# Performance work log

Measured on AMD Instinct MI355X. Metric: run time of the kernel, lower is better.

The kernel has to match this reference:

```python
import jax, jax.numpy as jnp
import numpy as np

B, S, D, H = 2, 2048, 2048, 16
HD = D // H  # 128


def _rope_tables(seq_len, dim, base=10000.0):
    inv_freq = 1.0 / (base ** (jnp.arange(0, dim, 2, dtype=jnp.float32) / dim))
    t = jnp.arange(seq_len, dtype=jnp.float32)
    freqs = jnp.outer(t, inv_freq)  # [S, dim/2]
    return jnp.cos(freqs), jnp.sin(freqs)


def _apply_rotary(x, cos, sin):
    # x: [B, S, H, HD]; cos/sin: [S, HD/2] -> broadcast [1, S, 1, HD/2]
    half = x.shape[-1] // 2
    x1, x2 = x[..., :half], x[..., half:]
    c = cos[None, :, None, :]
    s = sin[None, :, None, :]
    return jnp.concatenate([x1 * c - x2 * s, x1 * s + x2 * c], axis=-1)


def setup_inputs() -> dict:
    key = jax.random.key(0)
    ks = jax.random.split(key, 5)
    x = jax.random.normal(ks[0], (B, S, D), dtype=jnp.float32)
    Wq = jax.random.normal(ks[1], (D, D), dtype=jnp.float32) * 0.02
    Wk = jax.random.normal(ks[2], (D, D), dtype=jnp.float32) * 0.02
    Wv = jax.random.normal(ks[3], (D, D), dtype=jnp.float32) * 0.02
    Wo = jax.random.normal(ks[4], (D, D), dtype=jnp.float32) * 0.02
    mask = jnp.tril(jnp.ones((S, S), dtype=jnp.int32))[None, None]  # [1,1,S,S] causal
    return {"x": x, "mask": mask, "Wq": Wq, "Wk": Wk, "Wv": Wv, "Wo": Wo}


def reference(x, mask, Wq, Wk, Wv, Wo):
    b, s, d = x.shape
    # nn.Linear(bias=False): y = x @ W.T
    q = (x @ Wq.T).reshape(b, s, H, HD)
    k = (x @ Wk.T).reshape(b, s, H, HD)
    v = (x @ Wv.T).reshape(b, s, H, HD)
    cos, sin = _rope_tables(s, HD)
    q = _apply_rotary(q, cos, sin)
    k = _apply_rotary(k, cos, sin)
    # -> [B, H, S, HD]
    q = q.transpose(0, 2, 1, 3)
    k = k.transpose(0, 2, 1, 3)
    v = v.transpose(0, 2, 1, 3)
    scores = jnp.einsum('bhqd,bhkd->bhqk', q, k) / jnp.sqrt(jnp.float32(HD))
    scores = jnp.where(mask == 0, -jnp.inf, scores)
    attn = jax.nn.softmax(scores, axis=-1)
    out = jnp.einsum('bhqk,bhkd->bhqd', attn, v)
    out = out.transpose(0, 2, 1, 3).reshape(b, s, d)
    return out @ Wo.T
```

## Files before the change

### kernel.cpp

```cpp
#include <hip/hip_runtime.h>
#include <hip/hip_bf16.h>

typedef __attribute__((ext_vector_type(8))) short short8;
typedef __attribute__((ext_vector_type(4))) short s4;
typedef __attribute__((ext_vector_type(4))) float f32x4;

#define S_TOK 2048

__device__ __forceinline__ float b2f(ushort u) {
  union { unsigned i; float f; } v; v.i = ((unsigned)u) << 16; return v.f;
}
__device__ __forceinline__ ushort f2b(float f) {
  __hip_bfloat16 h = __float2bfloat16(f);
  union { __hip_bfloat16 h; ushort u; } v; v.h = h; return v.u;
}

__device__ __forceinline__ void async_load16(const void* g, void* l) {
  __builtin_amdgcn_global_load_lds(
      (const __attribute__((address_space(1))) unsigned int*)g,
      (__attribute__((address_space(3))) unsigned int*)l, 16, 0, 0);
}

__device__ __forceinline__ void wg_barrier() {
  __asm__ volatile("" ::: "memory");
  __builtin_amdgcn_s_barrier();
  __asm__ volatile("" ::: "memory");
}

__device__ const int QT_OF[40] = {0,1,2,3, 4,4,5,5,6,6,7,7, 8,8,8,9,9,9,10,10,10,11,11,11,
                                  12,12,12,12,13,13,13,13,14,14,14,14,15,15,15,15};
__device__ const int C_OF[40]  = {0,0,0,0, 0,1,0,1,0,1,0,1, 0,1,2,0,1,2,0,1,2,0,1,2,
                                  0,1,2,3,0,1,2,3,0,1,2,3,0,1,2,3};
__device__ const int S0_OF[16] = {0,1,2,3,4,6,8,10,12,15,18,21,24,28,32,36};
__device__ const int NC_OF[16] = {1,1,1,1,2,2,2,2,3,3,3,3,4,4,4,4};
__device__ const int SORD[40] = {3,4,6,8,10,11,12,13,15,16,18,19,21,22,23,24,25,26,28,29,
                                 30,32,33,34,36,37,38,39, 2,9,20,35, 1,7,17,31, 0,5,14,27};

__global__ __launch_bounds__(256) void cvt_f32_bf16(const float* __restrict__ in,
                                                    ushort* __restrict__ out, int n) {
  int i = (blockIdx.x * 256 + threadIdx.x) * 4;
  if (i < n) {
    float4 v = *(const float4*)(in + i);
    ushort4 o;
    o.x = f2b(v.x); o.y = f2b(v.y); o.z = f2b(v.z); o.w = f2b(v.w);
    *(ushort4*)(out + i) = o;
  }
}

__global__ __launch_bounds__(256) void cvt_w4(const float* __restrict__ w0,
                                              const float* __restrict__ w1,
                                              const float* __restrict__ w2,
                                              const float* __restrict__ w3,
                                              ushort* __restrict__ out, int n) {
  const float* src = blockIdx.y == 0 ? w0 : blockIdx.y == 1 ? w1 : blockIdx.y == 2 ? w2 : w3;
  int i = (blockIdx.x * 256 + threadIdx.x) * 4;
  if (i < n) {
    float4 v = *(const float4*)(src + i);
    ushort4 o;
    o.x = f2b(v.x); o.y = f2b(v.y); o.z = f2b(v.z); o.w = f2b(v.w);
    *(ushort4*)(out + (size_t)blockIdx.y * n + i) = o;
  }
}

template <bool OUTF32>
__global__ __launch_bounds__(512, 2) void gemm256(const ushort* __restrict__ A,
                                                  const ushort* __restrict__ Bw,
                                                  void* __restrict__ Cv,
                                                  int lda, int ldb, int ldc) {
  __shared__ __align__(16) ushort As[4][256 * 32];
  __shared__ __align__(16) ushort Bs[4][256 * 32];
  const int tid  = threadIdx.x;
  const int lane = tid & 63;
  const int w    = tid >> 6;
  const int quad = lane >> 4;
  const int l15  = lane & 15;
  const int m0 = blockIdx.x * 256;
  const int n0 = blockIdx.y * 256;
  const int wm = (w & 1) * 128;
  const int wn = (w >> 1) * 64;

  f32x4 acc[8][4];
  #pragma unroll
  for (int i = 0; i < 8; ++i)
    #pragma unroll
    for (int j = 0; j < 4; ++j) acc[i][j] = (f32x4){0.f, 0.f, 0.f, 0.f};

  auto stage = [&](int t, int j) {
    const int r = t & 3;
    const int s = tid + j * 512;
    const int row = s >> 2, qp = s & 3;
    const int kof = (qp ^ ((row >> 1) & 3)) * 8;
    const int k0 = t * 32;
    async_load16(A  + (size_t)(m0 + row) * lda + k0 + kof, &As[r][s * 8]);
    async_load16(Bw + (size_t)(n0 + row) * ldb + k0 + kof, &Bs[r][s * 8]);
  };

  stage(0, 0); stage(0, 1);
  stage(1, 0); stage(1, 1);
  stage(2, 0); stage(2, 1);
  __asm__ volatile("s_waitcnt vmcnt(8)" ::: "memory");
  wg_barrier();

  constexpr int nT = 64;
  #pragma unroll 1
  for (int u = 0; u < nT; ++u) {
    const ushort* At = As[u & 3];
    const ushort* Bt = Bs[u & 3];
    short8 afr[4], bfr[4];

    #pragma unroll
    for (int ni = 0; ni < 4; ++ni) {
      int row = wn + ni * 16 + l15;
      bfr[ni] = *(const short8*)&Bt[(row * 4 + (quad ^ ((row >> 1) & 3))) * 8];
    }
    #pragma unroll
    for (int mi = 0; mi < 4; ++mi) {
      int row = wm + mi * 16 + l15;
      afr[mi] = *(const short8*)&At[(row * 4 + (quad ^ ((row >> 1) & 3))) * 8];
    }
    if (u + 3 < nT) stage(u + 3, 0);
    wg_barrier();
    __asm__ volatile("s_waitcnt lgkmcnt(0)" ::: "memory");
    __builtin_amdgcn_s_setprio(1);
    #pragma unroll
    for (int mi = 0; mi < 4; ++mi)
      #pragma unroll
      for (int ni = 0; ni < 4; ++ni)
        acc[mi][ni] = __builtin_amdgcn_mfma_f32_16x16x32_bf16(afr[mi], bfr[ni], acc[mi][ni], 0, 0, 0);
    __builtin_amdgcn_s_setprio(0);
    wg_barrier();

    #pragma unroll
    for (int mi = 0; mi < 4; ++mi) {
      int row = wm + 64 + mi * 16 + l15;
      afr[mi] = *(const short8*)&At[(row * 4 + (quad ^ ((row >> 1) & 3))) * 8];
    }
    if (u + 3 < nT) stage(u + 3, 1);
    wg_barrier();
    __asm__ volatile("s_waitcnt lgkmcnt(0)" ::: "memory");
    __builtin_amdgcn_s_setprio(1);
    #pragma unroll
    for (int mi = 0; mi < 4; ++mi)
      #pragma unroll
      for (int ni = 0; ni < 4; ++ni)
        acc[4 + mi][ni] = __builtin_amdgcn_mfma_f32_16x16x32_bf16(afr[mi], bfr[ni], acc[4 + mi][ni], 0, 0, 0);
    __builtin_amdgcn_s_setprio(0);
    if (u + 3 < nT)      { __asm__ volatile("s_waitcnt vmcnt(8)" ::: "memory"); }
    else if (u + 2 < nT) { __asm__ volatile("s_waitcnt vmcnt(4)" ::: "memory"); }
    else if (u + 1 < nT) { __asm__ volatile("s_waitcnt vmcnt(0)" ::: "memory"); }
    wg_barrier();
  }

  #pragma unroll
  for (int mi = 0; mi < 8; ++mi)
    #pragma unroll
    for (int ni = 0; ni < 4; ++ni)
      #pragma unroll
      for (int r = 0; r < 4; ++r) {
        int rr = m0 + wm + mi * 16 + quad * 4 + r;
        int cc = n0 + wn + ni * 16 + l15;
        if constexpr (OUTF32)
          ((float*)Cv)[(size_t)rr * ldc + cc] = acc[mi][ni][r];
        else
          ((ushort*)Cv)[(size_t)rr * ldc + cc] = f2b(acc[mi][ni][r]);
      }
}

template <int BM, int BN, bool OUTF32>
__global__ __launch_bounds__(512, 2) void gemm_mn(const ushort* __restrict__ A,
                                                  const ushort* __restrict__ Bw,
                                                  void* __restrict__ Cv,
                                                  int lda, int ldb, int ldc) {
  constexpr int LA = BM / 128;
  constexpr int LB = BN / 128;
  constexpr int MI = BM / 32;
  constexpr int NI = BN / 64;
  static_assert(LA + LB == 3, "vmcnt literals assume 3 loads/thread/tile");
  __shared__ __align__(16) ushort As[4][BM * 32];
  __shared__ __align__(16) ushort Bs[4][BN * 32];
  const int tid  = threadIdx.x;
  const int lane = tid & 63;
  const int w    = tid >> 6;
  const int quad = lane >> 4;
  const int l15  = lane & 15;
  const int m0 = blockIdx.x * BM;
  const int n0 = blockIdx.y * BN;
  const int wm = (w & 1) * (BM / 2);
  const int wn = (w >> 1) * (BN / 4);

  f32x4 acc[MI][NI];
  #pragma unroll
  for (int i = 0; i < MI; ++i)
    #pragma unroll
    for (int j = 0; j < NI; ++j) acc[i][j] = (f32x4){0.f, 0.f, 0.f, 0.f};

  auto stage = [&](int t) {
    const int r = t & 3;
    const int k0 = t * 32;
    #pragma unroll
    for (int ja = 0; ja < LA; ++ja) {
      int s = tid + ja * 512;
      int row = s >> 2, qp = s & 3;
      int kof = (qp ^ ((row >> 1) & 3)) * 8;
      async_load16(A + (size_t)(m0 + row) * lda + k0 + kof, &As[r][s * 8]);
    }
    #pragma unroll
    for (int jb = 0; jb < LB; ++jb) {
      int s = tid + jb * 512;
      int row = s >> 2, qp = s & 3;
      int kof = (qp ^ ((row >> 1) & 3)) * 8;
      async_load16(Bw + (size_t)(n0 + row) * ldb + k0 + kof, &Bs[r][s * 8]);
    }
  };

  stage(0); stage(1); stage(2);
  __asm__ volatile("s_waitcnt vmcnt(6)" ::: "memory");
  wg_barrier();

  constexpr int nT = 64;
  #pragma unroll 1
  for (int u = 0; u < nT; ++u) {
    const ushort* At = As[u & 3];
    const ushort* Bt = Bs[u & 3];
    short8 afr[MI], bfr[NI];
    #pragma unroll
    for (int ni = 0; ni < NI; ++ni) {
      int row = wn + ni * 16 + l15;
      bfr[ni] = *(const short8*)&Bt[(row * 4 + (quad ^ ((row >> 1) & 3))) * 8];
    }
    #pragma unroll
    for (int mi = 0; mi < MI; ++mi) {
      int row = wm + mi * 16 + l15;
      afr[mi] = *(const short8*)&At[(row * 4 + (quad ^ ((row >> 1) & 3))) * 8];
    }
    if (u + 3 < nT) stage(u + 3);
    wg_barrier();
    __asm__ volatile("s_waitcnt lgkmcnt(0)" ::: "memory");
    __builtin_amdgcn_s_setprio(1);
    #pragma unroll
    for (int mi = 0; mi < MI; ++mi)
      #pragma unroll
      for (int ni = 0; ni < NI; ++ni)
        acc[mi][ni] = __builtin_amdgcn_mfma_f32_16x16x32_bf16(afr[mi], bfr[ni], acc[mi][ni], 0, 0, 0);
    __builtin_amdgcn_s_setprio(0);
    if (u + 3 < nT)      { __asm__ volatile("s_waitcnt vmcnt(6)" ::: "memory"); }
    else if (u + 2 < nT) { __asm__ volatile("s_waitcnt vmcnt(3)" ::: "memory"); }
    else if (u + 1 < nT) { __asm__ volatile("s_waitcnt vmcnt(0)" ::: "memory"); }
    wg_barrier();
  }

  #pragma unroll
  for (int mi = 0; mi < MI; ++mi)
    #pragma unroll
    for (int ni = 0; ni < NI; ++ni)
      #pragma unroll
      for (int r = 0; r < 4; ++r) {
        int rr = m0 + wm + mi * 16 + quad * 4 + r;
        int cc = n0 + wn + ni * 16 + l15;
        if constexpr (OUTF32)
          ((float*)Cv)[(size_t)rr * ldc + cc] = acc[mi][ni][r];
        else
          ((ushort*)Cv)[(size_t)rr * ldc + cc] = f2b(acc[mi][ni][r]);
      }
}

__global__ __launch_bounds__(256) void rope_k(ushort* __restrict__ QK) {
  const int t = blockIdx.x * 256 + threadIdx.x;
  const int j = t & 63;
  const int h = (t >> 6) & 15;
  const int row = t >> 10;
  const int pos = row & (S_TOK - 1);
  const float invf = __expf(-0.14391156831212787f * (float)j);
  const float ph = (float)pos * invf;
  float sn, cs;
  __sincosf(ph, &sn, &cs);
  size_t base = (size_t)row * 4096 + 2048 + h * 128 + j;
  float y1 = b2f(QK[base]);
  float y2 = b2f(QK[base + 64]);
  QK[base]      = f2b(y1 * cs - y2 * sn);
  QK[base + 64] = f2b(y1 * sn + y2 * cs);
}

__global__ __launch_bounds__(256, 2) void attn_chunk(const ushort* __restrict__ QK,
                                                     const ushort* __restrict__ Vt,
                                                     ushort* __restrict__ Opart,
                                                     float* __restrict__ Ml) {
  __shared__ __align__(16) ushort Ks[2][8192];
  __shared__ __align__(16) ushort Vs[2][8192];
  const int s = SORD[blockIdx.x];
  const int h = blockIdx.y, b = blockIdx.z;
  const int qt = QT_OF[s], c = C_OF[s];
  const int q0 = qt * 128;
  const int t0 = c * 8, tend = min(t0 + 8, 2 * qt + 2);
  const int slot = (b * 16 + h) * 40 + s;
  const int tid = threadIdx.x, lane = tid & 63, w = tid >> 6;
  const int quad = lane >> 4, l15 = lane & 15;
  const size_t rowbase = (size_t)b * S_TOK;
  const float scale = 0.08838834764831845f;

  short8 qf[2][4];
  #pragma unroll
  for (int m = 0; m < 2; ++m)
    #pragma unroll
    for (int ks = 0; ks < 4; ++ks)
      qf[m][ks] = *(const short8*)(QK + (rowbase + q0 + w * 32 + m * 16 + l15) * 4096
                                   + h * 128 + ks * 32 + quad * 8);

  #pragma unroll
  for (int m = 0; m < 2; ++m) {
    const int pos = (q0 + w * 32 + m * 16 + l15) & (S_TOK - 1);
    #pragma unroll
    for (int ks = 0; ks < 2; ++ks)
      #pragma unroll
      for (int j = 0; j < 8; ++j) {
        const int dj = ks * 32 + quad * 8 + j;
        const float ph = (float)pos * __expf(-0.14391156831212787f * (float)dj);
        float sn, cs;
        __sincosf(ph, &sn, &cs);
        const float x1 = b2f((ushort)qf[m][ks][j]);
        const float x2 = b2f((ushort)qf[m][ks + 2][j]);
        qf[m][ks][j]     = (short)f2b(x1 * cs - x2 * sn);
        qf[m][ks + 2][j] = (short)f2b(x1 * sn + x2 * cs);
      }
  }

  f32x4 o[2][8];
  #pragma unroll
  for (int m = 0; m < 2; ++m)
    #pragma unroll
    for (int no = 0; no < 8; ++no) o[m][no] = (f32x4){0.f, 0.f, 0.f, 0.f};
  float lsum[2] = {0.f, 0.f};

  auto issue_k = [&](int t, int buf) {
    const ushort* kb = QK + (rowbase + (size_t)t * 64) * 4096 + 2048 + h * 128;
    #pragma unroll
    for (int i = 0; i < 4; ++i) {
      int sl = tid + i * 256;
      int row = sl >> 4, cs = sl & 15;
      async_load16(kb + (size_t)row * 4096 + (cs ^ (row & 15)) * 8, &Ks[buf][sl * 8]);
    }
  };
  auto issue_v = [&](int t, int buf) {
    const ushort* vb = Vt + (size_t)(h * 128) * 4096 + b * S_TOK + (size_t)t * 64;
    #pragma unroll
    for (int i = 0; i < 4; ++i) {
      int sl = tid + i * 256;
      int hd = sl >> 3, cc = (sl & 7) ^ (hd & 7);
      async_load16(vb + (size_t)hd * 4096 + cc * 8, &Vs[buf][sl * 8]);
    }
  };

  issue_k(t0, 0);
  issue_v(t0, 0);

  for (int t = t0; t < tend; ++t) {
    const int buf = (t - t0) & 1;
    __syncthreads();
    if (t + 1 < tend) { issue_k(t + 1, buf ^ 1); issue_v(t + 1, buf ^ 1); }

    const ushort* KsT = Ks[buf];
    const ushort* VsT = Vs[buf];
    const bool domask = (t * 64 + 64 > q0);

    #pragma unroll
    for (int n = 0; n < 4; ++n) {
      short8 kf[4];
      #pragma unroll
      for (int ks = 0; ks < 4; ++ks) {
        int row = n * 16 + l15;
        kf[ks] = *(const short8*)&KsT[(row * 16 + ((ks * 4 + quad) ^ (row & 15))) * 8];
      }
      s4 pfm[2];
      #pragma unroll
      for (int m = 0; m < 2; ++m) {
        f32x4 z = (f32x4){0.f, 0.f, 0.f, 0.f};
        #pragma unroll
        for (int ks = 0; ks < 4; ++ks)
          z = __builtin_amdgcn_mfma_f32_16x16x32_bf16(kf[ks], qf[m][ks], z, 0, 0, 0);
        const int qg = q0 + w * 32 + m * 16 + l15;
        float p[4];
        #pragma unroll
        for (int r = 0; r < 4; ++r) {
          int kvg = t * 64 + n * 16 + quad * 4 + r;
          float pv = __expf(z[r] * scale);
          if (domask && kvg > qg) pv = 0.f;
          p[r] = pv;
          lsum[m] += pv;
        }
        s4 pk;
        pk[0] = (short)f2b(p[0]); pk[1] = (short)f2b(p[1]);
        pk[2] = (short)f2b(p[2]); pk[3] = (short)f2b(p[3]);
        pfm[m] = pk;
      }
      #pragma unroll
      for (int no = 0; no < 8; ++no) {
        int hd = no * 16 + l15;
        int cc = 2 * n + (quad >> 1);
        s4 vf = *(const s4*)&VsT[(hd * 8 + (cc ^ (hd & 7))) * 8 + (quad & 1) * 4];
        #pragma unroll
        for (int m = 0; m < 2; ++m)
          o[m][no] = __builtin_amdgcn_mfma_f32_16x16x16bf16_1k(pfm[m], vf, o[m][no], 0, 0, 0);
      }
    }
  }

  #pragma unroll
  for (int m = 0; m < 2; ++m) {
    lsum[m] += __shfl_xor(lsum[m], 16);
    lsum[m] += __shfl_xor(lsum[m], 32);
  }
  if (quad == 0) {
    #pragma unroll
    for (int m = 0; m < 2; ++m)
      Ml[(size_t)slot * 128 + w * 32 + m * 16 + l15] = lsum[m];
  }

  __syncthreads();
  ushort* Es = &Ks[0][w * 2048];
  ushort* Op = Opart + (size_t)slot * 16384;
  #pragma unroll
  for (int m = 0; m < 2; ++m) {
    #pragma unroll
    for (int no = 0; no < 8; ++no)
      #pragma unroll
      for (int r = 0; r < 4; ++r) {
        int rr = quad * 4 + r;
        int c8 = (no * 2 + (l15 >> 3)) ^ (rr & 7);
        Es[rr * 128 + c8 * 8 + (l15 & 7)] = f2b(o[m][no][r]);
      }
    __asm__ volatile("s_waitcnt lgkmcnt(0)" ::: "memory");
    #pragma unroll
    for (int j = 0; j < 4; ++j) {
      int cchunk = lane * 4 + j;
      int row_l = cchunk >> 4, colc = cchunk & 15;
      short8 vv = *(const short8*)&Es[row_l * 128 + (colc ^ (row_l & 7)) * 8];
      *(short8*)(Op + (size_t)(w * 32 + m * 16 + row_l) * 128 + colc * 8) = vv;
    }
    __asm__ volatile("s_waitcnt lgkmcnt(0)" ::: "memory");
  }
}

__global__ __launch_bounds__(256) void attn_combine(const ushort* __restrict__ Opart,
                                                    const float* __restrict__ Ml,
                                                    ushort* __restrict__ Ob) {
  const int qt = blockIdx.x, h = blockIdx.y, b = blockIdx.z;
  const int nc = NC_OF[qt];
  const int base = (b * 16 + h) * 40 + S0_OF[qt];
  const int tid = threadIdx.x;
  const int row = tid >> 1, half = tid & 1;

  float l = 0.f;
  for (int c = 0; c < nc; ++c) l += Ml[(size_t)(base + c) * 128 + row];
  const float inv_l = 1.f / l;

  float acc[64];
  #pragma unroll
  for (int i = 0; i < 64; ++i) acc[i] = 0.f;
  for (int c = 0; c < nc; ++c) {
    const ushort* Op = Opart + (size_t)(base + c) * 16384 + row * 128 + half * 64;
    #pragma unroll
    for (int k = 0; k < 8; ++k) {
      short8 v = *(const short8*)(Op + k * 8);
      #pragma unroll
      for (int u = 0; u < 8; ++u) acc[k * 8 + u] += b2f((ushort)v[u]);
    }
  }

  ushort* dst = Ob + ((size_t)(b * S_TOK + qt * 128 + row)) * 2048 + h * 128 + half * 64;
  #pragma unroll
  for (int k = 0; k < 8; ++k) {
    short8 ov;
    #pragma unroll
    for (int u = 0; u < 8; ++u) ov[u] = (short)f2b(acc[k * 8 + u] * inv_l);
    *(short8*)(dst + k * 8) = ov;
  }
}

extern "C" void kernel_launch(void* const* d_in, const int* in_sizes, int n_in,
                              void* d_out, int out_size, void* d_ws, size_t ws_size,
                              hipStream_t stream) {
  const float* x  = (const float*)d_in[0];
  const float* Wq = (const float*)d_in[2];
  const float* Wk = (const float*)d_in[3];
  const float* Wv = (const float*)d_in[4];
  const float* Wo = (const float*)d_in[5];
  float* out = (float*)d_out;

  ushort* xb    = (ushort*)d_ws;
  ushort* Wb    = xb + (size_t)4096 * 2048;
  ushort* QK    = Wb + (size_t)4 * 2048 * 2048;
  ushort* Vt    = QK + (size_t)4096 * 4096;
  ushort* Opart = Vt + (size_t)2048 * 4096;
  float*  Ml    = (float*)(Opart + (size_t)1280 * 16384);
  ushort* Ob    = xb;

  const int NX = 4096 * 2048;
  const int NW = 2048 * 2048;
  dim3 blk(256);
  dim3 blk512(512);

  cvt_f32_bf16<<<dim3(NX / 1024), blk, 0, stream>>>(x, xb, NX);
  cvt_w4<<<dim3(NW / 1024, 4), blk, 0, stream>>>(Wq, Wk, Wv, Wo, Wb, NW);

  gemm256<false><<<dim3(16, 16), blk512, 0, stream>>>(xb, Wb, QK, 2048, 2048, 4096);
  gemm_mn<128, 256, false><<<dim3(16, 16), blk512, 0, stream>>>(Wb + (size_t)2 * NW, xb, Vt,
                                                                2048, 2048, 4096);
  rope_k<<<dim3(16384), blk, 0, stream>>>(QK);
  attn_chunk<<<dim3(40, 16, 2), blk, 0, stream>>>(QK, Vt, Opart, Ml);
  attn_combine<<<dim3(16, 16, 2), blk, 0, stream>>>(Opart, Ml, Ob);
  gemm_mn<256, 128, true><<<dim3(16, 16), blk512, 0, stream>>>(Ob, Wb + (size_t)3 * NW, out,
                                                               2048, 2048, 2048);
}
```

Baseline: 411.5 us.

## Single-buffer V tile and split QK/PV phases to fit three blocks per CU

Drops the V double buffer to a single LDS tile and raises the occupancy target from two to three blocks per SM. The V tile for the current step is now loaded while QK^T and softmax run, and the next K tile is issued at the same time. Explicit vmcnt waits and barriers are placed before the PV phase and at the end of each iteration. This cuts LDS use so more blocks fit per CU, at the cost of an extra barrier per iteration, less prefetch distance for V, and more register pressure from holding all P fragments.

Result: slower. 475.3 us (+15.5%).

```diff
diff --git a/kernel.cpp b/kernel.cpp
--- a/kernel.cpp
+++ b/kernel.cpp
@@ -281,12 +281,12 @@
   QK[base + 64] = f2b(y1 * sn + y2 * cs);
 }
 
-__global__ __launch_bounds__(256, 2) void attn_chunk(const ushort* __restrict__ QK,
+__global__ __launch_bounds__(256, 3) void attn_chunk(const ushort* __restrict__ QK,
                                                      const ushort* __restrict__ Vt,
                                                      ushort* __restrict__ Opart,
                                                      float* __restrict__ Ml) {
   __shared__ __align__(16) ushort Ks[2][8192];
-  __shared__ __align__(16) ushort Vs[2][8192];
+  __shared__ __align__(16) ushort Vs[8192];
   const int s = SORD[blockIdx.x];
   const int h = blockIdx.y, b = blockIdx.z;
   const int qt = QT_OF[s], c = C_OF[s];
@@ -340,27 +340,30 @@
       async_load16(kb + (size_t)row * 4096 + (cs ^ (row & 15)) * 8, &Ks[buf][sl * 8]);
     }
   };
-  auto issue_v = [&](int t, int buf) {
+  auto issue_v = [&](int t) {
     const ushort* vb = Vt + (size_t)(h * 128) * 4096 + b * S_TOK + (size_t)t * 64;
     #pragma unroll
     for (int i = 0; i < 4; ++i) {
       int sl = tid + i * 256;
       int hd = sl >> 3, cc = (sl & 7) ^ (hd & 7);
-      async_load16(vb + (size_t)hd * 4096 + cc * 8, &Vs[buf][sl * 8]);
+      async_load16(vb + (size_t)hd * 4096 + cc * 8, &Vs[sl * 8]);
     }
   };
 
   issue_k(t0, 0);
-  issue_v(t0, 0);
+  __asm__ volatile("s_waitcnt vmcnt(0)" ::: "memory");
+  wg_barrier();
 
   for (int t = t0; t < tend; ++t) {
     const int buf = (t - t0) & 1;
-    __syncthreads();
-    if (t + 1 < tend) { issue_k(t + 1, buf ^ 1); issue_v(t + 1, buf ^ 1); }
+    const bool havek = (t + 1 < tend);
+
+    issue_v(t);
+    if (havek) issue_k(t + 1, buf ^ 1);
 
     const ushort* KsT = Ks[buf];
-    const ushort* VsT = Vs[buf];
     const bool domask = (t * 64 + 64 > q0);
+    s4 pfm[2][4];
 
     #pragma unroll
     for (int n = 0; n < 4; ++n) {
@@ -370,7 +373,6 @@
         int row = n * 16 + l15;
         kf[ks] = *(const short8*)&KsT[(row * 16 + ((ks * 4 + quad) ^ (row & 15))) * 8];
       }
-      s4 pfm[2];
       #pragma unroll
       for (int m = 0; m < 2; ++m) {
         f32x4 z = (f32x4){0.f, 0.f, 0.f, 0.f};
@@ -390,18 +392,27 @@
         s4 pk;
         pk[0] = (short)f2b(p[0]); pk[1] = (short)f2b(p[1]);
         pk[2] = (short)f2b(p[2]); pk[3] = (short)f2b(p[3]);
-        pfm[m] = pk;
-      }
+        pfm[m][n] = pk;
+      }
+    }
+    if (havek) { __asm__ volatile("s_waitcnt vmcnt(4)" ::: "memory"); }
+    else       { __asm__ volatile("s_waitcnt vmcnt(0)" ::: "memory"); }
+    wg_barrier();
+
+    #pragma unroll
+    for (int n = 0; n < 4; ++n) {
       #pragma unroll
       for (int no = 0; no < 8; ++no) {
         int hd = no * 16 + l15;
         int cc = 2 * n + (quad >> 1);
-        s4 vf = *(const s4*)&VsT[(hd * 8 + (cc ^ (hd & 7))) * 8 + (quad & 1) * 4];
+        s4 vf = *(const s4*)&Vs[(hd * 8 + (cc ^ (hd & 7))) * 8 + (quad & 1) * 4];
         #pragma unroll
         for (int m = 0; m < 2; ++m)
-          o[m][no] = __builtin_amdgcn_mfma_f32_16x16x16bf16_1k(pfm[m], vf, o[m][no], 0, 0, 0);
-      }
-    }
+          o[m][no] = __builtin_amdgcn_mfma_f32_16x16x16bf16_1k(pfm[m][n], vf, o[m][no], 0, 0, 0);
+      }
+    }
+    if (havek) { __asm__ volatile("s_waitcnt vmcnt(0)" ::: "memory"); }
+    wg_barrier();
   }
 
   #pragma unroll
```
